# Performance work log

Hardware: AMD Instinct MI355X
Metric: run time of the kernel (lower is better)

## Reference

```python
import jax, jax.numpy as jnp
import numpy as np

EPS = 1.0        # model eps for norm
STEP = 0.05      # step_size

def _norm(x):
    # torch: x / (eps + x.std(-1, keepdims=True)), torch std is unbiased (ddof=1)
    return x / (EPS + jnp.std(x, axis=-1, keepdims=True, ddof=1))

def setup_inputs() -> dict:
    key = jax.random.key(0)
    B, L, LM = 4, 512, 64
    G, E, K, D, KN = 32000, 256, 8, 6, 4
    ks = jax.random.split(key, 16)
    s = lambda k, shape, fan: (jax.random.normal(k, shape, jnp.float32) / np.sqrt(fan)).astype(jnp.float32)
    return dict(
        masked=jax.random.randint(ks[0], (B, L), 0, G),
        unmasked=jax.random.randint(ks[1], (B, L), 0, G),
        mask=jax.random.randint(ks[2], (B, LM), 0, L),
        embed=s(ks[3], (G, E), E),                 # embedding table
        Wt=s(ks[4], (D, E, E), E),                 # transition.weight per layer
        bt=jnp.zeros((D, E), jnp.float32),         # transition.bias per layer
        Wtc=s(ks[5], (D, E, E), E),                # transcore.weight per layer
        Wq=s(ks[6], (D, K * E, E), E),             # attq.weight per layer
        Wd=s(ks[7], (D, K * E, K * E), K * E),     # att_dense.weight per layer
        Wo=s(ks[8], (D, K * E, E), K * E),         # atto.weight per layer
        Wu=s(ks[9], (D, E, E), E),                 # updater.weight per layer
        Wem=s(ks[10], (E, E), E),                  # emittor.weight (head)
        Wkc=s(ks[11], (E * KN, E), E),             # kchoice.weight (head)
        bkc=jnp.zeros((E * KN,), jnp.float32),     # kchoice.bias (head)
    )

def reference(masked, unmasked, mask, embed, Wt, bt, Wtc, Wq, Wd, Wo, Wu, Wem, Wkc, bkc):
    B, L = masked.shape
    G, E = embed.shape
    K = Wq.shape[1] // E
    KN = Wkc.shape[0] // E
    inv_sqrt_e = 1.0 / np.sqrt(E)

    z = _norm(embed[masked])          # [B,L,E] input image
    xsa0 = z

    def step(xsa, p):
        wt, bt_, wtc, wq, wd, wo, wu = p
        # roll-based left/right transitions
        xsad = jax.nn.relu(jnp.roll(xsa, 1, axis=1) @ wt) @ wtc
        xsad = xsad + jax.nn.relu(jnp.roll(xsa, -1, axis=1) @ wtc.T) @ wt.T
        xsad = xsad + z @ wu.T + bt_   # use_input_image
        # QKV_Attention with kernel-expanded head dim: q [B,L,K,E] vs keys/values xsa [B,L,E]
        q = (xsa @ wq.T).reshape(B, L, K, E)
        h = jnp.einsum('blke,bme->blkm', q, xsa) * inv_sqrt_e
        pijk = jax.nn.softmax(h, axis=-1)
        y = jnp.einsum('blkm,bme->blke', pijk, xsa).reshape(B, L, K * E)
        # mode 1: Dense -> Relu -> Dense
        xid = jax.nn.relu(y @ wd.T) @ wo     # [B,L,E]
        xsad = _norm(xsad + xid)             # use_gradnorm
        xsa = _norm(xsa + STEP * xsad)       # use_layernorm
        return xsa, None

    xsa, _ = jax.lax.scan(step, xsa0, (Wt, bt, Wtc, Wq, Wd, Wo, Wu))

    # k-choice loss head (callback_cent)
    LM = mask.shape[1]
    lptok = jnp.take_along_axis(xsa, mask[:, :, None], axis=1)         # [B,LM,E]
    xx = (lptok @ Wkc.T + bkc).reshape(B, LM * KN, E)                  # kchoice
    xx = jnp.einsum('bnl,ble->bne', jnp.einsum('bne,ble->bnl', xx, xsa), xsa)
    logits = (xx @ Wem) @ embed.T                                      # [B,LM*KN,G]
    k_lp = jax.nn.log_softmax(logits, axis=-1).reshape(B, LM, KN, G)
    lptok = jax.scipy.special.logsumexp(k_lp, axis=2) - jnp.log(jnp.float32(KN))
    tgt = jnp.take_along_axis(unmasked, mask, axis=1)                  # [B,LM]
    cent = jnp.take_along_axis(lptok, tgt[:, :, None], axis=-1)[:, :, 0]
    return -cent.mean(-1)                                              # [B]
```

## Files before the change

kernel.cpp:

```cpp
#include <hip/hip_runtime.h>
#include <hip/hip_bf16.h>
#include <math.h>

typedef __bf16 bf16x8 __attribute__((ext_vector_type(8)));
typedef float floatx4 __attribute__((ext_vector_type(4)));

__device__ __forceinline__ short f2b(float f) {
  __hip_bfloat16 h = __float2bfloat16(f);
  return *reinterpret_cast<short*>(&h);
}
__device__ __forceinline__ float b2f(short s) {
  unsigned u = ((unsigned)(unsigned short)s) << 16;
  float f;
  __builtin_memcpy(&f, &u, 4);
  return f;
}

__device__ __forceinline__ void gl2lds16(const void* g, void* l) {
  __builtin_amdgcn_global_load_lds((__attribute__((address_space(1))) const void*)g,
                                   (__attribute__((address_space(3))) void*)l, 16, 0, 0);
}

__device__ __forceinline__ float block_sum(float v, float* sdata) {
#pragma unroll
  for (int o = 32; o > 0; o >>= 1) v += __shfl_down(v, o, 64);
  __syncthreads();
  int lane = threadIdx.x & 63, wid = threadIdx.x >> 6;
  if (lane == 0) sdata[wid] = v;
  __syncthreads();
  float s = 0.f;
  int nw = blockDim.x >> 6;
  for (int i = 0; i < nw; i++) s += sdata[i];
  return s;
}

__global__ void cvt_kernel(const float* __restrict__ src, short* __restrict__ dst, long n4) {
  long i = (long)blockIdx.x * blockDim.x + threadIdx.x;
  if (i < n4) {
    float4 v = ((const float4*)src)[i];
    short4 o;
    o.x = f2b(v.x); o.y = f2b(v.y); o.z = f2b(v.z); o.w = f2b(v.w);
    ((short4*)dst)[i] = o;
  }
}

__global__ void cvt2_kernel(const float* __restrict__ src, short* __restrict__ dst,
                            int ldS, int ldD, long sS, long sD) {
  src += (size_t)blockIdx.z * sS;
  dst += (size_t)blockIdx.z * sD;
  int c = blockIdx.x * 32 + threadIdx.x;
  int r0 = blockIdx.y * 32 + threadIdx.y;
#pragma unroll
  for (int i = 0; i < 32; i += 8)
    dst[(size_t)(r0 + i) * ldD + c] = f2b(src[(size_t)(r0 + i) * ldS + c]);
}

__global__ void cvtT2_kernel(const float* __restrict__ src, short* __restrict__ dst,
                             int ldS, int ldD, long sS, long sD) {
  src += (size_t)blockIdx.z * sS;
  dst += (size_t)blockIdx.z * sD;
  __shared__ float tile[32][33];
  int r0 = blockIdx.y * 32, c0 = blockIdx.x * 32;
  int tx = threadIdx.x, ty = threadIdx.y;
#pragma unroll
  for (int i = 0; i < 32; i += 8)
    tile[ty + i][tx] = src[(size_t)(r0 + ty + i) * ldS + c0 + tx];
  __syncthreads();
#pragma unroll
  for (int i = 0; i < 32; i += 8)
    dst[(size_t)(c0 + ty + i) * ldD + r0 + tx] = f2b(tile[tx][ty + i]);
}

__global__ void embed_norm_kernel(const int* __restrict__ masked,
                                  const float* __restrict__ embed,
                                  float* __restrict__ xsa, short* __restrict__ xsa_bf,
                                  short* __restrict__ xsaT_bf, short* __restrict__ catA,
                                  int E, int L, int ldA, int zoff) {
  int row = blockIdx.x;
  int g = masked[row];
  __shared__ float sdata[8];
  float x = embed[(size_t)g * E + threadIdx.x];
  float mean = block_sum(x, sdata) / E;
  float d = x - mean;
  float var = block_sum(d * d, sdata) / (E - 1);
  float val = x / (1.0f + sqrtf(var));
  size_t off = (size_t)row * E + threadIdx.x;
  xsa[off] = val;
  short b = f2b(val);
  xsa_bf[off] = b;
  catA[(size_t)row * ldA + zoff + threadIdx.x] = b;
  int bb = row / L, l = row - bb * L;
  xsaT_bf[((size_t)bb * E + threadIdx.x) * L + l] = b;
}

template <int BM, int BN, int OUT_BF16>
__global__ __launch_bounds__(256) void bgemm_kernel(
    const short* __restrict__ A, int lda, long sA,
    const short* __restrict__ B, int ldb, long sB,
    void* __restrict__ Cv, int ldc, long sC,
    int Ksz, float alpha, const float* __restrict__ bias,
    int relu, int shiftA, int shiftB, int nsplit, int Lroll) {
  constexpr int WM = BM / 2, WN = BN / 2;
  constexpr int MT = WM / 16, NT = WN / 16;
  constexpr int NCH = (BM + BN) * 8;
  constexpr int LPT = NCH / 256;
  A += (size_t)blockIdx.z * sA;
  B += (size_t)blockIdx.z * sB;
  float* Cf = (float*)Cv + (size_t)blockIdx.z * sC;
  short* Cb = (short*)Cv + (size_t)blockIdx.z * sC;
  int m0 = blockIdx.y * BM, n0 = blockIdx.x * BN;
  int shift = (n0 < nsplit) ? shiftA : shiftB;
  __shared__ short S[2][(BM + BN) * 64];
  int tid = threadIdx.x, lane = tid & 63, w = tid >> 6;
  int wm = (w & 1) * WM, wn = (w >> 1) * WN;
  int ml = lane & 15, q4 = lane >> 4, sw = ml & 7;

  const short* src[LPT];
#pragma unroll
  for (int i = 0; i < LPT; i++) {
    int q = i * 256 + w * 64 + lane;
    if (q < BM * 8) {
      int m = q >> 3, cl = q & 7, cs = cl ^ (m & 7);
      int mg = m0 + m;
      if (shift != 0) {
        int bb = mg / Lroll, l = mg - bb * Lroll;
        l = (l + shift + Lroll) % Lroll;
        mg = bb * Lroll + l;
      }
      src[i] = A + (size_t)mg * lda + cs * 8;
    } else {
      int qb = q - BM * 8;
      int n = qb >> 3, cl = qb & 7, cs = cl ^ (n & 7);
      src[i] = B + (size_t)(n0 + n) * ldb + cs * 8;
    }
  }
#pragma unroll
  for (int i = 0; i < LPT; i++)
    gl2lds16(src[i], &S[0][(i * 256 + w * 64) * 8]);
  floatx4 acc[MT][NT] = {};
  int nT = Ksz >> 6;
  for (int t = 0; t < nT; t++) {
    __syncthreads();
    int cur = t & 1;
    if (t + 1 < nT) {
      int nxt = cur ^ 1, ko = (t + 1) * 64;
#pragma unroll
      for (int i = 0; i < LPT; i++)
        gl2lds16(src[i] + ko, &S[nxt][(i * 256 + w * 64) * 8]);
    }
#pragma unroll
    for (int kk = 0; kk < 2; kk++) {
      int j = kk * 4 + q4;
      bf16x8 af[MT], bg[NT];
#pragma unroll
      for (int mt = 0; mt < MT; mt++) {
        int r = wm + mt * 16 + ml;
        af[mt] = *reinterpret_cast<const bf16x8*>(&S[cur][r * 64 + (j ^ sw) * 8]);
      }
#pragma unroll
      for (int nt = 0; nt < NT; nt++) {
        int r = wn + nt * 16 + ml;
        bg[nt] = *reinterpret_cast<const bf16x8*>(&S[cur][BM * 64 + r * 64 + (j ^ sw) * 8]);
      }
#pragma unroll
      for (int mt = 0; mt < MT; mt++)
#pragma unroll
        for (int nt = 0; nt < NT; nt++)
          acc[mt][nt] = __builtin_amdgcn_mfma_f32_16x16x32_bf16(af[mt], bg[nt], acc[mt][nt], 0, 0, 0);
    }
  }
#pragma unroll
  for (int mt = 0; mt < MT; mt++)
#pragma unroll
    for (int nt = 0; nt < NT; nt++) {
      floatx4 v = acc[mt][nt];
#pragma unroll
      for (int r = 0; r < 4; r++) {
        int grow = m0 + wm + mt * 16 + q4 * 4 + r;
        int gcol = n0 + wn + nt * 16 + ml;
        float x = alpha * v[r];
        if (bias) x += bias[gcol];
        if (relu) x = fmaxf(x, 0.f);
        if (OUT_BF16)
          Cb[(size_t)grow * ldc + gcol] = f2b(x);
        else
          Cf[(size_t)grow * ldc + gcol] = x;
      }
    }
}

__global__ void softmax_bf_kernel(short* __restrict__ h) {
  int lane = threadIdx.x & 63;
  size_t row = (size_t)blockIdx.x * 4 + (threadIdx.x >> 6);
  short* p = h + row * 512 + lane * 8;
  int4 raw = *(const int4*)p;
  short sh[8];
  __builtin_memcpy(sh, &raw, 16);
  float v[8];
  float m = -INFINITY;
#pragma unroll
  for (int i = 0; i < 8; i++) {
    v[i] = b2f(sh[i]);
    m = fmaxf(m, v[i]);
  }
#pragma unroll
  for (int o = 1; o < 64; o <<= 1) m = fmaxf(m, __shfl_xor(m, o, 64));
  float s = 0.f;
#pragma unroll
  for (int i = 0; i < 8; i++) {
    v[i] = expf(v[i] - m);
    s += v[i];
  }
#pragma unroll
  for (int o = 1; o < 64; o <<= 1) s += __shfl_xor(s, o, 64);
  float inv = 1.f / s;
#pragma unroll
  for (int i = 0; i < 8; i++) sh[i] = f2b(v[i] * inv);
  __builtin_memcpy(&raw, sh, 16);
  *(int4*)p = raw;
}

__global__ void addnorm_kernel(const float* __restrict__ xsadt,
                               float* __restrict__ xsa, short* __restrict__ xsa_bf,
                               short* __restrict__ xsaT_bf, int E, int L) {
  int row = blockIdx.x, t = threadIdx.x;
  __shared__ float sdata[8];
  size_t off = (size_t)row * E + t;
  float s1 = xsadt[off];
  float mean = block_sum(s1, sdata) / E;
  float d = s1 - mean;
  float var = block_sum(d * d, sdata) / (E - 1);
  float n1 = s1 / (1.f + sqrtf(var));
  float t2 = xsa[off] + 0.05f * n1;
  float mean2 = block_sum(t2, sdata) / E;
  float d2 = t2 - mean2;
  float var2 = block_sum(d2 * d2, sdata) / (E - 1);
  float res = t2 / (1.f + sqrtf(var2));
  xsa[off] = res;
  short b = f2b(res);
  xsa_bf[off] = b;
  int bb = row / L, l = row - bb * L;
  xsaT_bf[((size_t)bb * E + t) * L + l] = b;
}

__global__ void gather_kernel(const float* __restrict__ xsa, const int* __restrict__ mask,
                              const int* __restrict__ unmasked,
                              short* __restrict__ lptok_bf, int* __restrict__ tgt,
                              int L, int LM, int E) {
  int bi = blockIdx.x;
  int b = bi / LM;
  int pos = mask[bi];
  float v = xsa[((size_t)b * L + pos) * E + threadIdx.x];
  lptok_bf[(size_t)bi * E + threadIdx.x] = f2b(v);
  if (threadIdx.x == 0) tgt[bi] = unmasked[b * L + pos];
}

__global__ __launch_bounds__(256) void head_stats_kernel(
    const short* __restrict__ V, const short* __restrict__ Eb,
    float* __restrict__ stM, float* __restrict__ stS, int Ksz, int nch) {
  int m0 = blockIdx.y * 128, n0 = blockIdx.x * 128;
  __shared__ short As[2][8192];
  __shared__ short Bs[2][8192];
  int tid = threadIdx.x, lane = tid & 63, w = tid >> 6;
  int wm = (w & 1) * 64, wn = (w >> 1) * 64;
  int ml = lane & 15, q4 = lane >> 4, sw = ml & 7;
  const short* aSrc[4];
  const short* bSrc[4];
#pragma unroll
  for (int i = 0; i < 4; i++) {
    int q = i * 256 + w * 64 + lane;
    int m = q >> 3, cl = q & 7;
    int cs = cl ^ (m & 7);
    aSrc[i] = V + (size_t)(m0 + m) * Ksz + cs * 8;
    bSrc[i] = Eb + (size_t)(n0 + m) * Ksz + cs * 8;
  }
#pragma unroll
  for (int i = 0; i < 4; i++) {
    gl2lds16(aSrc[i], &As[0][(i * 256 + w * 64) * 8]);
    gl2lds16(bSrc[i], &Bs[0][(i * 256 + w * 64) * 8]);
  }
  floatx4 acc[4][4] = {};
  int nT = Ksz >> 6;
  for (int t = 0; t < nT; t++) {
    __syncthreads();
    int cur = t & 1;
    if (t + 1 < nT) {
      int nxt = cur ^ 1, ko = (t + 1) * 64;
#pragma unroll
      for (int i = 0; i < 4; i++) {
        gl2lds16(aSrc[i] + ko, &As[nxt][(i * 256 + w * 64) * 8]);
        gl2lds16(bSrc[i] + ko, &Bs[nxt][(i * 256 + w * 64) * 8]);
      }
    }
#pragma unroll
    for (int kk = 0; kk < 2; kk++) {
      int j = kk * 4 + q4;
      bf16x8 af[4], bg[4];
#pragma unroll
      for (int mt = 0; mt < 4; mt++) {
        int r = wm + mt * 16 + ml;
        af[mt] = *reinterpret_cast<const bf16x8*>(&As[cur][r * 64 + (j ^ sw) * 8]);
      }
#pragma unroll
      for (int nt = 0; nt < 4; nt++) {
        int r = wn + nt * 16 + ml;
        bg[nt] = *reinterpret_cast<const bf16x8*>(&Bs[cur][r * 64 + (j ^ sw) * 8]);
      }
#pragma unroll
      for (int mt = 0; mt < 4; mt++)
#pragma unroll
        for (int nt = 0; nt < 4; nt++)
          acc[mt][nt] = __builtin_amdgcn_mfma_f32_16x16x32_bf16(af[mt], bg[nt], acc[mt][nt], 0, 0, 0);
    }
  }
  __syncthreads();
  float (*sred)[2] = (float (*)[2]) & As[0][0];
  float (*sred2)[2] = (float (*)[2]) & Bs[0][0];
  float mx[4][4];
#pragma unroll
  for (int mt = 0; mt < 4; mt++)
#pragma unroll
    for (int r = 0; r < 4; r++)
      mx[mt][r] = fmaxf(fmaxf(acc[mt][0][r], acc[mt][1][r]), fmaxf(acc[mt][2][r], acc[mt][3][r]));
#pragma unroll
  for (int off = 1; off < 16; off <<= 1)
#pragma unroll
    for (int mt = 0; mt < 4; mt++)
#pragma unroll
      for (int r = 0; r < 4; r++) mx[mt][r] = fmaxf(mx[mt][r], __shfl_xor(mx[mt][r], off, 64));
  if (ml == 0)
#pragma unroll
    for (int mt = 0; mt < 4; mt++)
#pragma unroll
      for (int r = 0; r < 4; r++) sred[wm + mt * 16 + q4 * 4 + r][w >> 1] = mx[mt][r];
  __syncthreads();
  float sm[4][4];
#pragma unroll
  for (int mt = 0; mt < 4; mt++)
#pragma unroll
    for (int r = 0; r < 4; r++) {
      int row = wm + mt * 16 + q4 * 4 + r;
      float fm = fmaxf(sred[row][0], sred[row][1]);
      float s = 0.f;
#pragma unroll
      for (int nt = 0; nt < 4; nt++) s += expf(acc[mt][nt][r] - fm);
      sm[mt][r] = s;
    }
#pragma unroll
  for (int off = 1; off < 16; off <<= 1)
#pragma unroll
    for (int mt = 0; mt < 4; mt++)
#pragma unroll
      for (int r = 0; r < 4; r++) sm[mt][r] += __shfl_xor(sm[mt][r], off, 64);
  if (ml == 0)
#pragma unroll
    for (int mt = 0; mt < 4; mt++)
#pragma unroll
      for (int r = 0; r < 4; r++) sred2[wm + mt * 16 + q4 * 4 + r][w >> 1] = sm[mt][r];
  __syncthreads();
  if (tid < 128) {
    float fm = fmaxf(sred[tid][0], sred[tid][1]);
    stM[(size_t)(m0 + tid) * nch + blockIdx.x] = fm;
    stS[(size_t)(m0 + tid) * nch + blockIdx.x] = sred2[tid][0] + sred2[tid][1];
  }
}

__global__ void lse_reduce_kernel(const float* __restrict__ statsM,
                                  const float* __restrict__ statsS,
                                  float* __restrict__ lse, int nch) {
  int row = blockIdx.x, t = threadIdx.x;
  float m = -INFINITY, s = 0.f;
  for (int c = t; c < nch; c += blockDim.x) {
    float cm = statsM[(size_t)row * nch + c];
    float cs = statsS[(size_t)row * nch + c];
    float M = fmaxf(m, cm);
    s = s * expf(m - M) + cs * expf(cm - M);
    m = M;
  }
  __shared__ float sm[256], ss[256];
  sm[t] = m;
  ss[t] = s;
  __syncthreads();
  for (int o = 128; o > 0; o >>= 1) {
    if (t < o) {
      float m2 = sm[t + o], s2 = ss[t + o];
      float M = fmaxf(sm[t], m2);
      float sc = ss[t] * expf(sm[t] - M) + s2 * expf(m2 - M);
      sm[t] = M;
      ss[t] = sc;
    }
    __syncthreads();
  }
  if (t == 0) lse[row] = sm[0] + logf(ss[0]);
}

__global__ void logit_tgt_kernel(const short* __restrict__ V, const short* __restrict__ Eb,
                                 const int* __restrict__ tgt, float* __restrict__ lt,
                                 int E, int Nn, int KN, int LM) {
  int row = blockIdx.x;
  int b = row / Nn;
  int i = (row - b * Nn) / KN;
  int g = tgt[b * LM + i];
  __shared__ float sdata[8];
  float v = b2f(V[(size_t)row * E + threadIdx.x]) * b2f(Eb[(size_t)g * E + threadIdx.x]);
  float s = block_sum(v, sdata);
  if (threadIdx.x == 0) lt[row] = s;
}

__global__ void final_kernel(const float* __restrict__ lt, const float* __restrict__ lse,
                             float* __restrict__ out, int LM, int KN) {
  int b = blockIdx.x, i = threadIdx.x;
  int base = (b * LM + i) * KN;
  float m = -INFINITY;
  for (int k = 0; k < KN; k++) m = fmaxf(m, lt[base + k] - lse[base + k]);
  float s = 0.f;
  for (int k = 0; k < KN; k++) s += expf(lt[base + k] - lse[base + k] - m);
  float cent = m + logf(s) - logf((float)KN);
#pragma unroll
  for (int o = 32; o > 0; o >>= 1) cent += __shfl_down(cent, o, 64);
  if (i == 0) out[b] = -cent / LM;
}

static inline void bgemm(hipStream_t st, int cfg, const short* A, int lda, long sA,
                         const short* B, int ldb, long sB,
                         void* C, int ldc, long sC, int M, int N, int Ksz, int nb,
                         float alpha, const float* bias, int relu, int out_bf16,
                         int shiftA, int shiftB, int nsplit, int Lroll) {
  dim3 block(256);
  if (cfg == 0) {
    dim3 grid(N / 128, M / 128, nb);
    if (out_bf16)
      bgemm_kernel<128, 128, 1><<<grid, block, 0, st>>>(A, lda, sA, B, ldb, sB, C, ldc, sC, Ksz, alpha, bias, relu, shiftA, shiftB, nsplit, Lroll);
    else
      bgemm_kernel<128, 128, 0><<<grid, block, 0, st>>>(A, lda, sA, B, ldb, sB, C, ldc, sC, Ksz, alpha, bias, relu, shiftA, shiftB, nsplit, Lroll);
  } else if (cfg == 1) {
    dim3 grid(N / 64, M / 128, nb);
    if (out_bf16)
      bgemm_kernel<128, 64, 1><<<grid, block, 0, st>>>(A, lda, sA, B, ldb, sB, C, ldc, sC, Ksz, alpha, bias, relu, shiftA, shiftB, nsplit, Lroll);
    else
      bgemm_kernel<128, 64, 0><<<grid, block, 0, st>>>(A, lda, sA, B, ldb, sB, C, ldc, sC, Ksz, alpha, bias, relu, shiftA, shiftB, nsplit, Lroll);
  } else {
    dim3 grid(N / 64, M / 64, nb);
    if (out_bf16)
      bgemm_kernel<64, 64, 1><<<grid, block, 0, st>>>(A, lda, sA, B, ldb, sB, C, ldc, sC, Ksz, alpha, bias, relu, shiftA, shiftB, nsplit, Lroll);
    else
      bgemm_kernel<64, 64, 0><<<grid, block, 0, st>>>(A, lda, sA, B, ldb, sB, C, ldc, sC, Ksz, alpha, bias, relu, shiftA, shiftB, nsplit, Lroll);
  }
}

static inline void cvt(hipStream_t st, const float* src, short* dst, long n) {
  long n4 = n / 4;
  cvt_kernel<<<(int)((n4 + 255) / 256), 256, 0, st>>>(src, dst, n4);
}

static inline void cvt2(hipStream_t st, const float* src, short* dst, int R, int C,
                        int ldS, int ldD, long sS, long sD, int nb) {
  dim3 grid(C / 32, R / 32, nb), block(32, 8);
  cvt2_kernel<<<grid, block, 0, st>>>(src, dst, ldS, ldD, sS, sD);
}

static inline void cvtT2(hipStream_t st, const float* src, short* dst, int R, int C,
                         int ldS, int ldD, long sS, long sD, int nb) {
  dim3 grid(C / 32, R / 32, nb), block(32, 8);
  cvtT2_kernel<<<grid, block, 0, st>>>(src, dst, ldS, ldD, sS, sD);
}

extern "C" void kernel_launch(void* const* d_in, const int* in_sizes, int n_in,
                              void* d_out, int out_size, void* d_ws, size_t ws_size,
                              hipStream_t stream) {
  const int* masked = (const int*)d_in[0];
  const int* unmasked = (const int*)d_in[1];
  const int* mask = (const int*)d_in[2];
  const float* embed = (const float*)d_in[3];
  const float* Wt = (const float*)d_in[4];
  const float* bt = (const float*)d_in[5];
  const float* Wtc = (const float*)d_in[6];
  const float* Wq = (const float*)d_in[7];
  const float* Wd = (const float*)d_in[8];
  const float* Wo = (const float*)d_in[9];
  const float* Wu = (const float*)d_in[10];
  const float* Wem = (const float*)d_in[11];
  const float* Wkc = (const float*)d_in[12];
  const float* bkc = (const float*)d_in[13];

  const int B = out_size;
  const int BL = in_sizes[0];
  const int L = BL / B;
  const int BLM = in_sizes[2];
  const int LM = BLM / B;
  const int E = in_sizes[4] / in_sizes[5];
  const int D = in_sizes[5] / E;
  const int G = in_sizes[3] / E;
  const int K = in_sizes[7] / (D * E * E);
  const int KN = in_sizes[12] / (E * E);
  const int KE = K * E;
  const int N = LM * KN;
  const float inv_sqrt_e = 1.0f / sqrtf((float)E);
  const int nch = G / 128;
  const int E3 = 3 * E;
  const int KA = E3 + KE;

  char* base = (char*)d_ws;
  size_t off = 0;
  auto carve = [&](size_t bytes) {
    char* p = base + off;
    off += (bytes + 255) & ~(size_t)255;
    return p;
  };
  float* xsa = (float*)carve((size_t)BL * E * 4);
  float* xsad = (float*)carve((size_t)BL * E * 4);
  float* stM = (float*)carve((size_t)B * N * nch * 4);
  float* stS = (float*)carve((size_t)B * N * nch * 4);
  float* lse = (float*)carve((size_t)B * N * 4);
  float* lt = (float*)carve((size_t)B * N * 4);
  int* tgt = (int*)carve((size_t)B * LM * 4);
  short* xsa_bf = (short*)carve((size_t)BL * E * 2);
  short* xsaT_bf = (short*)carve((size_t)B * E * L * 2);
  short* catA = (short*)carve((size_t)BL * KA * 2);
  short* qy_bf = (short*)carve((size_t)BL * KE * 2);
  short* hP_bf = (short*)carve((size_t)B * L * K * L * 2);
  short* wd_all = (short*)carve((size_t)D * KE * KE * 2);
  short* wq_all = (short*)carve((size_t)D * KE * E * 2);
  short* Bcat1 = (short*)carve((size_t)D * 2 * E * E * 2);
  short* Bcat2x = (short*)carve((size_t)D * E * KA * 2);
  short* embed_bf = (short*)carve((size_t)G * E * 2);
  short* WemT_bf = (short*)carve((size_t)E * E * 2);
  short* Wkc_bf = (short*)carve((size_t)KN * E * E * 2);
  short* gram_bf = (short*)carve((size_t)B * E * E * 2);
  short* xx_bf = (short*)carve((size_t)B * N * E * 2);
  short* xx2_bf = (short*)carve((size_t)B * N * E * 2);
  short* vv_bf = (short*)carve((size_t)B * N * E * 2);
  short* lptok_bf = (short*)carve((size_t)BLM * E * 2);

  cvt(stream, embed, embed_bf, (long)G * E);
  cvt(stream, Wd, wd_all, (long)D * KE * KE);
  cvt(stream, Wq, wq_all, (long)D * KE * E);
  cvt(stream, Wkc, Wkc_bf, (long)KN * E * E);
  cvtT2(stream, Wem, WemT_bf, E, E, E, E, 0, 0, 1);
  cvtT2(stream, Wt, Bcat1, E, E, E, E, (long)E * E, (long)2 * E * E, D);
  cvt2(stream, Wtc, Bcat1 + (size_t)E * E, E, E, E, E, (long)E * E, (long)2 * E * E, D);
  cvtT2(stream, Wtc, Bcat2x, E, E, E, KA, (long)E * E, (long)E * KA, D);
  cvt2(stream, Wt, Bcat2x + E, E, E, E, KA, (long)E * E, (long)E * KA, D);
  cvt2(stream, Wu, Bcat2x + 2 * E, E, E, E, KA, (long)E * E, (long)E * KA, D);
  cvtT2(stream, Wo, Bcat2x + E3, KE, E, E, KA, (long)KE * E, (long)E * KA, D);

  embed_norm_kernel<<<BL, E, 0, stream>>>(masked, embed, xsa, xsa_bf, xsaT_bf, catA,
                                          E, L, KA, 2 * E);

  for (int d = 0; d < D; d++) {
    const float* btl = bt + (size_t)d * E;
    bgemm(stream, 2, xsa_bf, E, 0, Bcat1 + (size_t)d * 2 * E * E, E, 0,
          catA, KA, 0, BL, 2 * E, E, 1, 1.f, nullptr, 1, 1, -1, +1, E, L);
    bgemm(stream, 1, xsa_bf, E, 0, wq_all + (size_t)d * KE * E, E, 0,
          qy_bf, KE, 0, BL, KE, E, 1, 1.f, nullptr, 0, 1, 0, 0, 0, L);
    bgemm(stream, 0, qy_bf, E, (long)L * KE, xsa_bf, E, (long)L * E,
          hP_bf, L, (long)L * K * L, L * K, L, E, B, inv_sqrt_e, nullptr, 0, 1, 0, 0, 0, L);
    softmax_bf_kernel<<<B * L * K / 4, 256, 0, stream>>>(hP_bf);
    bgemm(stream, 1, hP_bf, L, (long)L * K * L, xsaT_bf, L, (long)E * L,
          qy_bf, E, (long)L * KE, L * K, E, L, B, 1.f, nullptr, 0, 1, 0, 0, 0, L);
    bgemm(stream, 1, qy_bf, KE, 0, wd_all + (size_t)d * KE * KE, KE, 0,
          catA + E3, KA, 0, BL, KE, KE, 1, 1.f, nullptr, 1, 1, 0, 0, 0, L);
    bgemm(stream, 2, catA, KA, 0, Bcat2x + (size_t)d * E * KA, KA, 0,
          xsad, E, 0, BL, E, KA, 1, 1.f, btl, 0, 0, 0, 0, 0, L);
    addnorm_kernel<<<BL, E, 0, stream>>>(xsad, xsa, xsa_bf, xsaT_bf, E, L);
  }

  gather_kernel<<<BLM, E, 0, stream>>>(xsa, mask, unmasked, lptok_bf, tgt, L, LM, E);
  bgemm(stream, 2, xsaT_bf, L, (long)E * L, xsaT_bf, L, (long)E * L,
        gram_bf, E, (long)E * E, E, E, L, B, 1.f, nullptr, 0, 1, 0, 0, 0, L);
  bgemm(stream, 2, lptok_bf, E, 0, Wkc_bf, E, 0, xx_bf, KN * E, 0, BLM, KN * E, E, 1,
        1.f, bkc, 0, 1, 0, 0, 0, L);
  bgemm(stream, 2, xx_bf, E, (long)N * E, gram_bf, E, (long)E * E,
        xx2_bf, E, (long)N * E, N, E, E, B, 1.f, nullptr, 0, 1, 0, 0, 0, L);
  bgemm(stream, 2, xx2_bf, E, 0, WemT_bf, E, 0, vv_bf, E, 0, B * N, E, E, 1,
        1.f, nullptr, 0, 1, 0, 0, 0, L);
  head_stats_kernel<<<dim3(nch, (B * N) / 128), 256, 0, stream>>>(vv_bf, embed_bf, stM, stS, E, nch);
  lse_reduce_kernel<<<B * N, 256, 0, stream>>>(stM, stS, lse, nch);
  logit_tgt_kernel<<<B * N, E, 0, stream>>>(vv_bf, embed_bf, tgt, lt, E, N, KN, LM);
  final_kernel<<<B, LM, 0, stream>>>(lt, lse, (float*)d_out, LM, KN);
}
```

Before: 929.9 us.

## Fuse softmax into attention GEMMs and merge transition with query projection

The separate softmax kernel is removed. The score GEMM now applies exp in its epilogue without subtracting a max. The following P·V GEMM computes row sums with an extra MFMA against a ones vector and divides by them in its epilogue. The transition and Wq projections are also concatenated into a single GEMM launch, with a second output zone writing the query columns. This saves kernel launches and a full read/write pass over the large attention matrix. The risks are overflow in the unstabilised exp and extra MFMA work for the row sums.

```diff
diff --git a/kernel.cpp b/kernel.cpp
--- a/kernel.cpp
+++ b/kernel.cpp
@@ -93,13 +93,14 @@
   xsaT_bf[((size_t)bb * E + threadIdx.x) * L + l] = b;
 }
 
-template <int BM, int BN, int OUT_BF16>
+template <int BM, int BN, int OUT_BF16, int ASUM>
 __global__ __launch_bounds__(256) void bgemm_kernel(
     const short* __restrict__ A, int lda, long sA,
     const short* __restrict__ B, int ldb, long sB,
     void* __restrict__ Cv, int ldc, long sC,
+    short* __restrict__ C2b, int ldc2, int ncut,
     int Ksz, float alpha, const float* __restrict__ bias,
-    int relu, int shiftA, int shiftB, int nsplit, int Lroll) {
+    int relu, int expo, int shiftA, int shiftB, int ns1, int ns2, int Lroll) {
   constexpr int WM = BM / 2, WN = BN / 2;
   constexpr int MT = WM / 16, NT = WN / 16;
   constexpr int NCH = (BM + BN) * 8;
@@ -109,7 +110,8 @@
   float* Cf = (float*)Cv + (size_t)blockIdx.z * sC;
   short* Cb = (short*)Cv + (size_t)blockIdx.z * sC;
   int m0 = blockIdx.y * BM, n0 = blockIdx.x * BN;
-  int shift = (n0 < nsplit) ? shiftA : shiftB;
+  int shift = (n0 < ns1) ? shiftA : ((n0 < ns2) ? shiftB : 0);
+  int zone2 = (C2b != nullptr) && (n0 >= ncut);
   __shared__ short S[2][(BM + BN) * 64];
   int tid = threadIdx.x, lane = tid & 63, w = tid >> 6;
   int wm = (w & 1) * WM, wn = (w >> 1) * WN;
@@ -138,6 +140,10 @@
   for (int i = 0; i < LPT; i++)
     gl2lds16(src[i], &S[0][(i * 256 + w * 64) * 8]);
   floatx4 acc[MT][NT] = {};
+  floatx4 sumacc[ASUM ? MT : 1] = {};
+  bf16x8 ones;
+#pragma unroll
+  for (int i = 0; i < 8; i++) ones[i] = (__bf16)1.0f;
   int nT = Ksz >> 6;
   for (int t = 0; t < nT; t++) {
     __syncthreads();
@@ -167,10 +173,19 @@
 #pragma unroll
         for (int nt = 0; nt < NT; nt++)
           acc[mt][nt] = __builtin_amdgcn_mfma_f32_16x16x32_bf16(af[mt], bg[nt], acc[mt][nt], 0, 0, 0);
-    }
-  }
-#pragma unroll
-  for (int mt = 0; mt < MT; mt++)
+      if (ASUM)
+#pragma unroll
+        for (int mt = 0; mt < MT; mt++)
+          sumacc[mt] = __builtin_amdgcn_mfma_f32_16x16x32_bf16(af[mt], ones, sumacc[mt], 0, 0, 0);
+    }
+  }
+#pragma unroll
+  for (int mt = 0; mt < MT; mt++) {
+    float sinv[4];
+    if (ASUM) {
+#pragma unroll
+      for (int r = 0; r < 4; r++) sinv[r] = 1.f / sumacc[mt][r];
+    }
 #pragma unroll
     for (int nt = 0; nt < NT; nt++) {
       floatx4 v = acc[mt][nt];
@@ -179,45 +194,21 @@
         int grow = m0 + wm + mt * 16 + q4 * 4 + r;
         int gcol = n0 + wn + nt * 16 + ml;
         float x = alpha * v[r];
+        if (ASUM) x *= sinv[r];
         if (bias) x += bias[gcol];
-        if (relu) x = fmaxf(x, 0.f);
-        if (OUT_BF16)
-          Cb[(size_t)grow * ldc + gcol] = f2b(x);
-        else
+        if (relu && !zone2) x = fmaxf(x, 0.f);
+        if (expo) x = expf(x);
+        if (OUT_BF16) {
+          if (zone2)
+            C2b[(size_t)grow * ldc2 + (gcol - ncut)] = f2b(x);
+          else
+            Cb[(size_t)grow * ldc + gcol] = f2b(x);
+        } else {
           Cf[(size_t)grow * ldc + gcol] = x;
-      }
-    }
-}
-
-__global__ void softmax_bf_kernel(short* __restrict__ h) {
-  int lane = threadIdx.x & 63;
-  size_t row = (size_t)blockIdx.x * 4 + (threadIdx.x >> 6);
-  short* p = h + row * 512 + lane * 8;
-  int4 raw = *(const int4*)p;
-  short sh[8];
-  __builtin_memcpy(sh, &raw, 16);
-  float v[8];
-  float m = -INFINITY;
-#pragma unroll
-  for (int i = 0; i < 8; i++) {
-    v[i] = b2f(sh[i]);
-    m = fmaxf(m, v[i]);
-  }
-#pragma unroll
-  for (int o = 1; o < 64; o <<= 1) m = fmaxf(m, __shfl_xor(m, o, 64));
-  float s = 0.f;
-#pragma unroll
-  for (int i = 0; i < 8; i++) {
-    v[i] = expf(v[i] - m);
-    s += v[i];
-  }
-#pragma unroll
-  for (int o = 1; o < 64; o <<= 1) s += __shfl_xor(s, o, 64);
-  float inv = 1.f / s;
-#pragma unroll
-  for (int i = 0; i < 8; i++) sh[i] = f2b(v[i] * inv);
-  __builtin_memcpy(&raw, sh, 16);
-  *(int4*)p = raw;
+        }
+      }
+    }
+  }
 }
 
 __global__ void addnorm_kernel(const float* __restrict__ xsadt,
@@ -425,27 +416,35 @@
                          const short* B, int ldb, long sB,
                          void* C, int ldc, long sC, int M, int N, int Ksz, int nb,
                          float alpha, const float* bias, int relu, int out_bf16,
-                         int shiftA, int shiftB, int nsplit, int Lroll) {
+                         int shiftA, int shiftB, int ns1, int ns2, int Lroll,
+                         int expo = 0, int asum = 0,
+                         short* C2 = nullptr, int ldc2 = 0, int ncut = 0) {
   dim3 block(256);
+#define BG_ARGS A, lda, sA, B, ldb, sB, C, ldc, sC, C2, ldc2, ncut, Ksz, alpha, bias, relu, expo, shiftA, shiftB, ns1, ns2, Lroll
   if (cfg == 0) {
     dim3 grid(N / 128, M / 128, nb);
     if (out_bf16)
-      bgemm_kernel<128, 128, 1><<<grid, block, 0, st>>>(A, lda, sA, B, ldb, sB, C, ldc, sC, Ksz, alpha, bias, relu, shiftA, shiftB, nsplit, Lroll);
+      bgemm_kernel<128, 128, 1, 0><<<grid, block, 0, st>>>(BG_ARGS);
     else
-      bgemm_kernel<128, 128, 0><<<grid, block, 0, st>>>(A, lda, sA, B, ldb, sB, C, ldc, sC, Ksz, alpha, bias, relu, shiftA, shiftB, nsplit, Lroll);
+      bgemm_kernel<128, 128, 0, 0><<<grid, block, 0, st>>>(BG_ARGS);
   } else if (cfg == 1) {
     dim3 grid(N / 64, M / 128, nb);
-    if (out_bf16)
-      bgemm_kernel<128, 64, 1><<<grid, block, 0, st>>>(A, lda, sA, B, ldb, sB, C, ldc, sC, Ksz, alpha, bias, relu, shiftA, shiftB, nsplit, Lroll);
-    else
-      bgemm_kernel<128, 64, 0><<<grid, block, 0, st>>>(A, lda, sA, B, ldb, sB, C, ldc, sC, Ksz, alpha, bias, relu, shiftA, shiftB, nsplit, Lroll);
+    if (out_bf16) {
+      if (asum)
+        bgemm_kernel<128, 64, 1, 1><<<grid, block, 0, st>>>(BG_ARGS);
+      else
+        bgemm_kernel<128, 64, 1, 0><<<grid, block, 0, st>>>(BG_ARGS);
+    } else {
+      bgemm_kernel<128, 64, 0, 0><<<grid, block, 0, st>>>(BG_ARGS);
+    }
   } else {
     dim3 grid(N / 64, M / 64, nb);
     if (out_bf16)
-      bgemm_kernel<64, 64, 1><<<grid, block, 0, st>>>(A, lda, sA, B, ldb, sB, C, ldc, sC, Ksz, alpha, bias, relu, shiftA, shiftB, nsplit, Lroll);
+      bgemm_kernel<64, 64, 1, 0><<<grid, block, 0, st>>>(BG_ARGS);
     else
-      bgemm_kernel<64, 64, 0><<<grid, block, 0, st>>>(A, lda, sA, B, ldb, sB, C, ldc, sC, Ksz, alpha, bias, relu, shiftA, shiftB, nsplit, Lroll);
-  }
+      bgemm_kernel<64, 64, 0, 0><<<grid, block, 0, st>>>(BG_ARGS);
+  }
+#undef BG_ARGS
 }
 
 static inline void cvt(hipStream_t st, const float* src, short* dst, long n) {
@@ -499,6 +498,7 @@
   const int nch = G / 128;
   const int E3 = 3 * E;
   const int KA = E3 + KE;
+  const int NQ = 2 * E + KE;
 
   char* base = (char*)d_ws;
   size_t off = 0;
@@ -520,8 +520,7 @@
   short* qy_bf = (short*)carve((size_t)BL * KE * 2);
   short* hP_bf = (short*)carve((size_t)B * L * K * L * 2);
   short* wd_all = (short*)carve((size_t)D * KE * KE * 2);
-  short* wq_all = (short*)carve((size_t)D * KE * E * 2);
-  short* Bcat1 = (short*)carve((size_t)D * 2 * E * E * 2);
+  short* BcatQ = (short*)carve((size_t)D * NQ * E * 2);
   short* Bcat2x = (short*)carve((size_t)D * E * KA * 2);
   short* embed_bf = (short*)carve((size_t)G * E * 2);
   short* WemT_bf = (short*)carve((size_t)E * E * 2);
@@ -534,11 +533,11 @@
 
   cvt(stream, embed, embed_bf, (long)G * E);
   cvt(stream, Wd, wd_all, (long)D * KE * KE);
-  cvt(stream, Wq, wq_all, (long)D * KE * E);
   cvt(stream, Wkc, Wkc_bf, (long)KN * E * E);
   cvtT2(stream, Wem, WemT_bf, E, E, E, E, 0, 0, 1);
-  cvtT2(stream, Wt, Bcat1, E, E, E, E, (long)E * E, (long)2 * E * E, D);
-  cvt2(stream, Wtc, Bcat1 + (size_t)E * E, E, E, E, E, (long)E * E, (long)2 * E * E, D);
+  cvtT2(stream, Wt, BcatQ, E, E, E, E, (long)E * E, (long)NQ * E, D);
+  cvt2(stream, Wtc, BcatQ + (size_t)E * E, E, E, E, E, (long)E * E, (long)NQ * E, D);
+  cvt2(stream, Wq, BcatQ + (size_t)2 * E * E, KE, E, E, E, (long)KE * E, (long)NQ * E, D);
   cvtT2(stream, Wtc, Bcat2x, E, E, E, KA, (long)E * E, (long)E * KA, D);
   cvt2(stream, Wt, Bcat2x + E, E, E, E, KA, (long)E * E, (long)E * KA, D);
   cvt2(stream, Wu, Bcat2x + 2 * E, E, E, E, KA, (long)E * E, (long)E * KA, D);
@@ -549,31 +548,31 @@
 
   for (int d = 0; d < D; d++) {
     const float* btl = bt + (size_t)d * E;
-    bgemm(stream, 2, xsa_bf, E, 0, Bcat1 + (size_t)d * 2 * E * E, E, 0,
-          catA, KA, 0, BL, 2 * E, E, 1, 1.f, nullptr, 1, 1, -1, +1, E, L);
-    bgemm(stream, 1, xsa_bf, E, 0, wq_all + (size_t)d * KE * E, E, 0,
-          qy_bf, KE, 0, BL, KE, E, 1, 1.f, nullptr, 0, 1, 0, 0, 0, L);
+    bgemm(stream, 1, xsa_bf, E, 0, BcatQ + (size_t)d * NQ * E, E, 0,
+          catA, KA, 0, BL, NQ, E, 1, 1.f, nullptr, 1, 1,
+          -1, +1, E, 2 * E, L, 0, 0, qy_bf, KE, 2 * E);
     bgemm(stream, 0, qy_bf, E, (long)L * KE, xsa_bf, E, (long)L * E,
-          hP_bf, L, (long)L * K * L, L * K, L, E, B, inv_sqrt_e, nullptr, 0, 1, 0, 0, 0, L);
-    softmax_bf_kernel<<<B * L * K / 4, 256, 0, stream>>>(hP_bf);
+          hP_bf, L, (long)L * K * L, L * K, L, E, B, inv_sqrt_e, nullptr, 0, 1,
+          0, 0, 0, 0, L, 1);
     bgemm(stream, 1, hP_bf, L, (long)L * K * L, xsaT_bf, L, (long)E * L,
-          qy_bf, E, (long)L * KE, L * K, E, L, B, 1.f, nullptr, 0, 1, 0, 0, 0, L);
+          qy_bf, E, (long)L * KE, L * K, E, L, B, 1.f, nullptr, 0, 1,
+          0, 0, 0, 0, L, 0, 1);
     bgemm(stream, 1, qy_bf, KE, 0, wd_all + (size_t)d * KE * KE, KE, 0,
-          catA + E3, KA, 0, BL, KE, KE, 1, 1.f, nullptr, 1, 1, 0, 0, 0, L);
+          catA + E3, KA, 0, BL, KE, KE, 1, 1.f, nullptr, 1, 1, 0, 0, 0, 0, L);
     bgemm(stream, 2, catA, KA, 0, Bcat2x + (size_t)d * E * KA, KA, 0,
-          xsad, E, 0, BL, E, KA, 1, 1.f, btl, 0, 0, 0, 0, 0, L);
+          xsad, E, 0, BL, E, KA, 1, 1.f, btl, 0, 0, 0, 0, 0, 0, L);
     addnorm_kernel<<<BL, E, 0, stream>>>(xsad, xsa, xsa_bf, xsaT_bf, E, L);
   }
 
   gather_kernel<<<BLM, E, 0, stream>>>(xsa, mask, unmasked, lptok_bf, tgt, L, LM, E);
   bgemm(stream, 2, xsaT_bf, L, (long)E * L, xsaT_bf, L, (long)E * L,
-        gram_bf, E, (long)E * E, E, E, L, B, 1.f, nullptr, 0, 1, 0, 0, 0, L);
+        gram_bf, E, (long)E * E, E, E, L, B, 1.f, nullptr, 0, 1, 0, 0, 0, 0, L);
   bgemm(stream, 2, lptok_bf, E, 0, Wkc_bf, E, 0, xx_bf, KN * E, 0, BLM, KN * E, E, 1,
-        1.f, bkc, 0, 1, 0, 0, 0, L);
+        1.f, bkc, 0, 1, 0, 0, 0, 0, L);
   bgemm(stream, 2, xx_bf, E, (long)N * E, gram_bf, E, (long)E * E,
-        xx2_bf, E, (long)N * E, N, E, E, B, 1.f, nullptr, 0, 1, 0, 0, 0, L);
+        xx2_bf, E, (long)N * E, N, E, E, B, 1.f, nullptr, 0, 1, 0, 0, 0, 0, L);
   bgemm(stream, 2, xx2_bf, E, 0, WemT_bf, E, 0, vv_bf, E, 0, B * N, E, E, 1,
-        1.f, nullptr, 0, 1, 0, 0, 0, L);
+        1.f, nullptr, 0, 1, 0, 0, 0, 0, L);
   head_stats_kernel<<<dim3(nch, (B * N) / 128), 256, 0, stream>>>(vv_bf, embed_bf, stM, stS, E, nch);
   lse_reduce_kernel<<<B * N, 256, 0, stream>>>(stM, stS, lse, nch);
   logit_tgt_kernel<<<B * N, E, 0, stream>>>(vv_bf, embed_bf, tgt, lt, E, N, KN, LM);
```

Result: no change. 939.2 us (+1.0%).
